# Optimization experiments

Hardware: AMD Instinct MI355X
Metric: run time of the kernel (lower is better)

## Reference

```python
import jax, jax.numpy as jnp
import numpy as np

N = 120000   # hits
K = 512      # non-noise objects (ids 1..K; id 0 = noise)
D = 8        # cluster-space dim
C = 6        # pid classes
Q_MIN = 1.0
NOISE_THR = 0
PAYLOAD_W = 1.0
EPS = 1e-9


def setup_inputs() -> dict:
    key = jax.random.key(0)
    ks = jax.random.split(key, 9)
    beta = jax.random.uniform(ks[0], (N,), dtype=jnp.float32) * 0.95 + 0.01  # keep arctanh finite
    x = jax.random.normal(ks[1], (N, D), dtype=jnp.float32)
    object_id = jax.random.randint(ks[2], (N,), 0, K + 1).astype(jnp.int32)
    # guarantee every object id (and noise id 0) appears at least once
    object_id = object_id.at[: K + 1].set(jnp.arange(K + 1, dtype=jnp.int32))
    energy = jax.random.normal(ks[3], (N,), dtype=jnp.float32)
    energy_per_hit = jax.random.normal(ks[4], (N,), dtype=jnp.float32)
    momentum = jax.random.normal(ks[5], (N, 3), dtype=jnp.float32)
    momentum_per_hit = jax.random.normal(ks[6], (N, 3), dtype=jnp.float32)
    pid_logits = jax.random.normal(ks[7], (N, C), dtype=jnp.float32)
    pid_per_hit = jax.random.randint(ks[8], (N,), 0, C).astype(jnp.int32)
    return dict(beta=beta, x=x, object_id=object_id, energy=energy,
                energy_per_hit=energy_per_hit, momentum=momentum,
                momentum_per_hit=momentum_per_hit, pid_logits=pid_logits,
                pid_per_hit=pid_per_hit)


def _oc_core(beta, x, object_id):
    """condensation_loss_tiger with weights=1, max_n_rep=0 (no repulsive sampling)."""
    oids = jnp.arange(1, K + 1, dtype=object_id.dtype)
    att_mask = object_id[:, None] == oids[None, :]              # [N, K]
    q = jnp.arctanh(beta) ** 2 + Q_MIN                          # [N]
    alphas = jnp.argmax(q[:, None] * att_mask, axis=0)          # [K] condensation points
    x_k = x[alphas]                                             # [K, D]
    q_k = q[alphas]                                             # [K]
    # squared euclidean distance via gemm (avoids [N,K,D] intermediate)
    d2 = (jnp.sum(x * x, axis=1)[:, None] + jnp.sum(x_k * x_k, axis=1)[None, :]
          - 2.0 * (x @ x_k.T))
    d2 = jnp.maximum(d2, 0.0)                                   # [N, K]
    dist = jnp.sqrt(jnp.maximum(d2, 1e-12))
    qw = q[:, None] * q_k[None, :]                              # [N, K]
    # attractive: per-object normalized by hits in object, then mean over objects
    att_norm = jnp.sum(att_mask, axis=0).astype(x.dtype)        # [K]
    v_att = jnp.sum(jnp.where(att_mask, qw * d2, 0.0) / (att_norm + EPS)[None, :]) / K
    # repulsive: hinge (1 - dist), normalized by n_hits not in object
    rep_mask = (~att_mask) & (dist < 1.0)
    n_rep_k = jnp.sum(~att_mask, axis=0).astype(x.dtype)        # [K]
    n_rep = jnp.sum(rep_mask)
    v_rep = jnp.sum(jnp.where(rep_mask, qw * (1.0 - dist), 0.0) / (n_rep_k + EPS)[None, :]) / K
    l_coward = jnp.mean(1.0 - beta[alphas])
    noise_m = (object_id <= NOISE_THR).astype(beta.dtype)
    l_noise = jnp.sum(beta * noise_m) / jnp.sum(noise_m)
    return v_att, v_rep, l_coward, l_noise, n_rep


def reference(beta, x, object_id, energy, energy_per_hit, momentum,
              momentum_per_hit, pid_logits, pid_per_hit):
    v_att, v_rep, l_coward, l_noise, n_rep = _oc_core(beta, x, object_id)
    oc_total = v_att + v_rep + l_coward + l_noise
    # payload losses on non-noise hits (masked means == F.*_loss on gathered rows)
    m = (object_id > NOISE_THR).astype(beta.dtype)              # [N]
    nm = jnp.sum(m)
    e_loss = jnp.sum((energy - energy_per_hit) ** 2 * m) / nm
    p_loss = jnp.sum((momentum - momentum_per_hit) ** 2 * m[:, None]) / (nm * momentum.shape[1])
    logp = jax.nn.log_softmax(pid_logits, axis=-1)              # [N, C]
    nll = -jnp.take_along_axis(logp, pid_per_hit[:, None], axis=1)[:, 0]
    pid_loss = jnp.sum(nll * m) / nm
    total = oc_total + PAYLOAD_W * (e_loss + p_loss + pid_loss)
    return (v_att, v_rep, l_coward, l_noise, n_rep.astype(jnp.float32),
            oc_total, e_loss, p_loss, pid_loss, total)
```

## Files before the change

### kernel.cpp

```cpp
#include <hip/hip_runtime.h>
#include <math.h>

#define KOBJ 512
#define KTW 12
#define TK 64
#define NTILE (KOBJ / TK)
#define HB 4
#define HCH (256 * HB)

__device__ __forceinline__ float wave_red_f(float v) {
  #pragma unroll
  for (int off = 32; off > 0; off >>= 1) v += __shfl_down(v, off, 64);
  return v;
}

__device__ __forceinline__ float q_of_beta(float b) {
  float a = 0.5f * __logf((1.f + b) / (1.f - b));
  return fmaf(a, a, 1.f);
}

__global__ __launch_bounds__(256) void
k_prep(const float* __restrict__ beta, const int* __restrict__ oid,
       const float* __restrict__ energy, const float* __restrict__ eph,
       const float* __restrict__ mom, const float* __restrict__ mph,
       const float* __restrict__ logits, const int* __restrict__ pid,
       unsigned long long* __restrict__ amax_part,
       unsigned* __restrict__ cnt_part,
       float* __restrict__ scal_part, int n, int M) {
  __shared__ unsigned long long lmax[KOBJ];
  __shared__ unsigned lcnt[KOBJ];
  for (int t = threadIdx.x; t < KOBJ; t += 256) { lmax[t] = 0ull; lcnt[t] = 0u; }
  __syncthreads();

  float e_t = 0.f, p_t = 0.f, pid_t = 0.f, noise_t = 0.f, ncnt = 0.f, mcnt = 0.f;
  for (int i = blockIdx.x * 256 + threadIdx.x; i < n; i += M * 256) {
    float b = beta[i];
    int o = oid[i];
    if (o > 0) {
      float q = q_of_beta(b);
      unsigned long long key = ((unsigned long long)__float_as_uint(q) << 32)
                             | (unsigned long long)(unsigned)(~(unsigned)i);
      atomicMax(&lmax[o - 1], key);
      atomicAdd(&lcnt[o - 1], 1u);
      mcnt += 1.f;
      float de = energy[i] - eph[i];
      e_t = fmaf(de, de, e_t);
      float p0 = mom[3*i+0] - mph[3*i+0];
      float p1 = mom[3*i+1] - mph[3*i+1];
      float p2 = mom[3*i+2] - mph[3*i+2];
      p_t = fmaf(p0, p0, p_t); p_t = fmaf(p1, p1, p_t); p_t = fmaf(p2, p2, p_t);
      const float* lg = logits + 6*i;
      float l0=lg[0], l1=lg[1], l2=lg[2], l3=lg[3], l4=lg[4], l5=lg[5];
      float mx = fmaxf(fmaxf(fmaxf(l0,l1),fmaxf(l2,l3)), fmaxf(l4,l5));
      float s = __expf(l0-mx)+__expf(l1-mx)+__expf(l2-mx)
              + __expf(l3-mx)+__expf(l4-mx)+__expf(l5-mx);
      int pc = pid[i];
      float lp = (pc==0)?l0:(pc==1)?l1:(pc==2)?l2:(pc==3)?l3:(pc==4)?l4:l5;
      pid_t += mx + __logf(s) - lp;
    } else {
      noise_t += b;
      ncnt += 1.f;
    }
  }
  __syncthreads();

  for (int t = threadIdx.x; t < KOBJ; t += 256) {
    amax_part[(size_t)blockIdx.x * KOBJ + t] = lmax[t];
    cnt_part[(size_t)blockIdx.x * KOBJ + t]  = lcnt[t];
  }

  float vals[6] = {e_t, p_t, pid_t, noise_t, ncnt, mcnt};
  #pragma unroll
  for (int j = 0; j < 6; j++) vals[j] = wave_red_f(vals[j]);
  __shared__ float sred[4][6];
  int w = threadIdx.x >> 6, l = threadIdx.x & 63;
  if (l == 0) {
    #pragma unroll
    for (int j = 0; j < 6; j++) sred[w][j] = vals[j];
  }
  __syncthreads();
  if (threadIdx.x == 0) {
    #pragma unroll
    for (int j = 0; j < 6; j++)
      scal_part[blockIdx.x * 8 + j] = sred[0][j]+sred[1][j]+sred[2][j]+sred[3][j];
  }
}

__global__ __launch_bounds__(256) void
k_gather(const float* __restrict__ x, const float* __restrict__ beta,
         const unsigned long long* __restrict__ amax_part,
         const unsigned* __restrict__ cnt_part,
         float* __restrict__ ktab, float* __restrict__ cow_part, int n, int M) {
  int ko = threadIdx.x & 63;
  int chunk = threadIdx.x >> 6;
  int k = blockIdx.x * 64 + ko;
  int m0 = (chunk * M) >> 2, m1 = ((chunk + 1) * M) >> 2;

  unsigned long long key = 0ull;
  unsigned cnt = 0u;
  for (int m = m0; m < m1; m++) {
    unsigned long long km = amax_part[(size_t)m * KOBJ + k];
    key = (km > key) ? km : key;
    cnt += cnt_part[(size_t)m * KOBJ + k];
  }
  __shared__ unsigned long long skey[4][64];
  __shared__ unsigned scnt[4][64];
  skey[chunk][ko] = key;
  scnt[chunk][ko] = cnt;
  __syncthreads();

  float cow = 0.f;
  if (chunk == 0) {
    #pragma unroll
    for (int c = 1; c < 4; c++) {
      unsigned long long kc = skey[c][ko];
      key = (kc > key) ? kc : key;
      cnt += scnt[c][ko];
    }
    unsigned idx = ~(unsigned)(key & 0xffffffffull);
    float q_k = __uint_as_float((unsigned)(key >> 32));
    const float4* xp = (const float4*)x;
    float4 xa = xp[2 * (size_t)idx];
    float4 xb = xp[2 * (size_t)idx + 1];
    float xv[8] = {xa.x, xa.y, xa.z, xa.w, xb.x, xb.y, xb.z, xb.w};
    float s2 = 0.f;
    #pragma unroll
    for (int c = 0; c < 8; c++) s2 = fmaf(xv[c], xv[c], s2);
    float* kt = ktab + (size_t)k * KTW;
    #pragma unroll
    for (int c = 0; c < 8; c++) kt[c] = xv[c];
    kt[8]  = s2;
    kt[9]  = q_k / ((float)(n - (int)cnt) + 1e-9f);
    kt[10] = q_k / ((float)cnt + 1e-9f);
    kt[11] = 0.f;
    cow = 1.f - beta[idx];
    cow = wave_red_f(cow);
    if (ko == 0) cow_part[blockIdx.x] = cow;
  }
}

__global__ __launch_bounds__(256) void
k_pairs(const float* __restrict__ x, const float* __restrict__ beta,
        const int* __restrict__ oid, const float* __restrict__ ktab,
        float* __restrict__ pairs_part, int n) {
  __shared__ float skt[TK * KTW];
  const int tile0 = blockIdx.y * TK;
  for (int t = threadIdx.x; t < TK * KTW; t += 256)
    skt[t] = ktab[(size_t)tile0 * KTW + t];
  __syncthreads();

  float yi[HB][8], b2[HB], qi[HB];
  int own[HB];
  const float4* xp = (const float4*)x;
  #pragma unroll
  for (int h = 0; h < HB; h++) {
    int i = blockIdx.x * HCH + h * 256 + threadIdx.x;
    if (i < n) {
      float4 xa = xp[2 * (size_t)i];
      float4 xb = xp[2 * (size_t)i + 1];
      float xi[8] = {xa.x, xa.y, xa.z, xa.w, xb.x, xb.y, xb.z, xb.w};
      float s = 0.f;
      #pragma unroll
      for (int c = 0; c < 8; c++) {
        s = fmaf(xi[c], xi[c], s);
        yi[h][c] = -2.f * xi[c];
      }
      b2[h] = s;
      qi[h] = q_of_beta(beta[i]);
      own[h] = oid[i] - 1 - tile0;
    } else {
      #pragma unroll
      for (int c = 0; c < 8; c++) yi[h][c] = 0.f;
      b2[h] = 3.f;
      qi[h] = 0.f;
      own[h] = -1;
    }
  }

  float att = 0.f, rep = 0.f, nrep = 0.f;
  #pragma unroll 2
  for (int k = 0; k < TK; k++) {
    const float* kt = &skt[k * KTW];
    float k0 = kt[0], k1 = kt[1], k2 = kt[2], k3 = kt[3];
    float k4 = kt[4], k5 = kt[5], k6 = kt[6], k7 = kt[7];
    float s2 = kt[8], wr = kt[9];
    #pragma unroll
    for (int h = 0; h < HB; h++) {
      float d2 = b2[h] + s2;
      d2 = fmaf(yi[h][0], k0, d2);
      d2 = fmaf(yi[h][1], k1, d2);
      d2 = fmaf(yi[h][2], k2, d2);
      d2 = fmaf(yi[h][3], k3, d2);
      d2 = fmaf(yi[h][4], k4, d2);
      d2 = fmaf(yi[h][5], k5, d2);
      d2 = fmaf(yi[h][6], k6, d2);
      d2 = fmaf(yi[h][7], k7, d2);
      if (d2 < 1.f) {
        float dist = sqrtf(fmaxf(d2, 1e-12f));
        rep = fmaf(qi[h] * (1.f - dist), wr, rep);
        nrep += 1.f;
      }
    }
  }

  #pragma unroll
  for (int h = 0; h < HB; h++) {
    int ko = own[h];
    if (ko >= 0 && ko < TK) {
      const float* kt = &skt[ko * KTW];
      float d2 = b2[h] + kt[8];
      #pragma unroll
      for (int c = 0; c < 8; c++) d2 = fmaf(yi[h][c], kt[c], d2);
      att = fmaf(qi[h] * fmaxf(d2, 0.f), kt[10], att);
      if (d2 < 1.f) {
        float dist = sqrtf(fmaxf(d2, 1e-12f));
        rep = fmaf(-qi[h] * (1.f - dist), kt[9], rep);
        nrep -= 1.f;
      }
    }
  }

  att = wave_red_f(att);
  rep = wave_red_f(rep);
  nrep = wave_red_f(nrep);
  __shared__ float sred[4][3];
  int w = threadIdx.x >> 6, l = threadIdx.x & 63;
  if (l == 0) { sred[w][0] = att; sred[w][1] = rep; sred[w][2] = nrep; }
  __syncthreads();
  if (threadIdx.x == 0) {
    int bid = blockIdx.y * gridDim.x + blockIdx.x;
    pairs_part[bid * 4 + 0] = sred[0][0]+sred[1][0]+sred[2][0]+sred[3][0];
    pairs_part[bid * 4 + 1] = sred[0][1]+sred[1][1]+sred[2][1]+sred[3][1];
    pairs_part[bid * 4 + 2] = sred[0][2]+sred[1][2]+sred[2][2]+sred[3][2];
  }
}

__global__ __launch_bounds__(256) void
k_finalize(const float* __restrict__ pairs_part, int nblk_tot,
           const float* __restrict__ scal_part, int M,
           const float* __restrict__ cow_part, float* __restrict__ out) {
  float v[9] = {0,0,0,0,0,0,0,0,0};
  for (int b = threadIdx.x; b < nblk_tot; b += 256) {
    v[0] += pairs_part[b * 4 + 0];
    v[1] += pairs_part[b * 4 + 1];
    v[2] += pairs_part[b * 4 + 2];
  }
  for (int m = threadIdx.x; m < M; m += 256) {
    #pragma unroll
    for (int j = 0; j < 6; j++) v[3 + j] += scal_part[m * 8 + j];
  }
  #pragma unroll
  for (int j = 0; j < 9; j++) v[j] = wave_red_f(v[j]);
  __shared__ float sred[4][9];
  int w = threadIdx.x >> 6, l = threadIdx.x & 63;
  if (l == 0) {
    #pragma unroll
    for (int j = 0; j < 9; j++) sred[w][j] = v[j];
  }
  __syncthreads();
  if (threadIdx.x == 0) {
    float t[9];
    #pragma unroll
    for (int j = 0; j < 9; j++) t[j] = sred[0][j]+sred[1][j]+sred[2][j]+sred[3][j];
    float cow = cow_part[0]+cow_part[1]+cow_part[2]+cow_part[3]
              + cow_part[4]+cow_part[5]+cow_part[6]+cow_part[7];
    float v_att  = t[0] / (float)KOBJ;
    float v_rep  = t[1] / (float)KOBJ;
    float n_rep  = t[2];
    float l_cow  = cow / (float)KOBJ;
    float l_noise = t[6] / t[7];
    float oc = v_att + v_rep + l_cow + l_noise;
    float nm = t[8];
    float e_loss  = t[3] / nm;
    float p_loss  = t[4] / (nm * 3.f);
    float pid_loss = t[5] / nm;
    out[0] = v_att;
    out[1] = v_rep;
    out[2] = l_cow;
    out[3] = l_noise;
    out[4] = n_rep;
    out[5] = oc;
    out[6] = e_loss;
    out[7] = p_loss;
    out[8] = pid_loss;
    out[9] = oc + e_loss + p_loss + pid_loss;
  }
}

extern "C" void kernel_launch(void* const* d_in, const int* in_sizes, int n_in,
                              void* d_out, int out_size, void* d_ws, size_t ws_size,
                              hipStream_t stream) {
  const float* beta   = (const float*)d_in[0];
  const float* x      = (const float*)d_in[1];
  const int*   oid    = (const int*)d_in[2];
  const float* energy = (const float*)d_in[3];
  const float* eph    = (const float*)d_in[4];
  const float* mom    = (const float*)d_in[5];
  const float* mph    = (const float*)d_in[6];
  const float* logits = (const float*)d_in[7];
  const int*   pid    = (const int*)d_in[8];
  float* out = (float*)d_out;
  const int n = in_sizes[0];
  const int nhb = (n + HCH - 1) / HCH;
  const int nblk_tot = nhb * NTILE;

  char* base = (char*)d_ws;
  size_t off = 0;
  float* ktab       = (float*)(base + off); off += (size_t)KOBJ * KTW * 4;
  float* cow_part   = (float*)(base + off); off += 8 * 4;
  float* pairs_part = (float*)(base + off); off += (size_t)nblk_tot * 4 * 4;
  off = (off + 255) & ~(size_t)255;

  size_t per_m = (size_t)KOBJ * 8 + (size_t)KOBJ * 4 + 32;
  long long avail = (long long)ws_size - (long long)off;
  int M = (int)(avail / (long long)per_m);
  if (M > 256) M = 256;
  M &= ~3;
  if (M < 4) M = 4;

  unsigned long long* amax_part = (unsigned long long*)(base + off); off += (size_t)M * KOBJ * 8;
  unsigned* cnt_part = (unsigned*)(base + off);                      off += (size_t)M * KOBJ * 4;
  float* scal_part   = (float*)(base + off);                         off += (size_t)M * 8 * 4;

  k_prep<<<M, 256, 0, stream>>>(beta, oid, energy, eph, mom, mph, logits, pid,
                                amax_part, cnt_part, scal_part, n, M);
  k_gather<<<8, 256, 0, stream>>>(x, beta, amax_part, cnt_part, ktab, cow_part, n, M);
  k_pairs<<<dim3(nhb, NTILE), 256, 0, stream>>>(x, beta, oid, ktab, pairs_part, n);
  k_finalize<<<1, 256, 0, stream>>>(pairs_part, nblk_tot, scal_part, M, cow_part, out);
}
```

Baseline: 127.4 us.

## Fuse all phases into one cooperative persistent kernel with grid syncs

Replaces the four separate launches (prep, gather, pairs, finalize) with one cooperative kernel of 512 blocks that separates the phases with grid.sync, and falls back to separate launches if the cooperative launch fails. It also raises prep parallelism to 512 blocks, spreads gather over 64 blocks, and turns the pair tiles into a grid-stride loop. The aim is to cut launch gaps and idle tail time between stages. In exchange it adds grid-barrier cost, must fit two blocks per CU, reloads the k-tile into shared memory for every work item, and makes gather reduce over more partials.

```diff
diff --git a/kernel.cpp b/kernel.cpp
--- a/kernel.cpp
+++ b/kernel.cpp
@@ -1,5 +1,8 @@
 #include <hip/hip_runtime.h>
+#include <hip/hip_cooperative_groups.h>
 #include <math.h>
+
+namespace cg = cooperative_groups;
 
 #define KOBJ 512
 #define KTW 12
@@ -7,6 +10,9 @@
 #define NTILE (KOBJ / TK)
 #define HB 4
 #define HCH (256 * HB)
+#define MPREP 512
+#define GGATH 64
+#define GRID 512
 
 __device__ __forceinline__ float wave_red_f(float v) {
   #pragma unroll
@@ -19,21 +25,20 @@
   return fmaf(a, a, 1.f);
 }
 
-__global__ __launch_bounds__(256) void
-k_prep(const float* __restrict__ beta, const int* __restrict__ oid,
-       const float* __restrict__ energy, const float* __restrict__ eph,
-       const float* __restrict__ mom, const float* __restrict__ mph,
-       const float* __restrict__ logits, const int* __restrict__ pid,
-       unsigned long long* __restrict__ amax_part,
-       unsigned* __restrict__ cnt_part,
-       float* __restrict__ scal_part, int n, int M) {
-  __shared__ unsigned long long lmax[KOBJ];
-  __shared__ unsigned lcnt[KOBJ];
-  for (int t = threadIdx.x; t < KOBJ; t += 256) { lmax[t] = 0ull; lcnt[t] = 0u; }
+__device__ __forceinline__ void
+phase_prep(const float* __restrict__ beta, const int* __restrict__ oid,
+           const float* __restrict__ energy, const float* __restrict__ eph,
+           const float* __restrict__ mom, const float* __restrict__ mph,
+           const float* __restrict__ logits, const int* __restrict__ pid,
+           unsigned long long* __restrict__ amax_part,
+           unsigned* __restrict__ cnt_part, float* __restrict__ scal_part,
+           int n, int bid, int tid,
+           unsigned long long* lmax, unsigned* lcnt, float (*sred)[10]) {
+  for (int t = tid; t < KOBJ; t += 256) { lmax[t] = 0ull; lcnt[t] = 0u; }
   __syncthreads();
 
   float e_t = 0.f, p_t = 0.f, pid_t = 0.f, noise_t = 0.f, ncnt = 0.f, mcnt = 0.f;
-  for (int i = blockIdx.x * 256 + threadIdx.x; i < n; i += M * 256) {
+  for (int i = bid * 256 + tid; i < n; i += MPREP * 256) {
     float b = beta[i];
     int o = oid[i];
     if (o > 0) {
@@ -64,58 +69,55 @@
   }
   __syncthreads();
 
-  for (int t = threadIdx.x; t < KOBJ; t += 256) {
-    amax_part[(size_t)blockIdx.x * KOBJ + t] = lmax[t];
-    cnt_part[(size_t)blockIdx.x * KOBJ + t]  = lcnt[t];
+  for (int t = tid; t < KOBJ; t += 256) {
+    amax_part[(size_t)bid * KOBJ + t] = lmax[t];
+    cnt_part[(size_t)bid * KOBJ + t]  = lcnt[t];
   }
 
   float vals[6] = {e_t, p_t, pid_t, noise_t, ncnt, mcnt};
   #pragma unroll
   for (int j = 0; j < 6; j++) vals[j] = wave_red_f(vals[j]);
-  __shared__ float sred[4][6];
-  int w = threadIdx.x >> 6, l = threadIdx.x & 63;
+  int w = tid >> 6, l = tid & 63;
   if (l == 0) {
     #pragma unroll
     for (int j = 0; j < 6; j++) sred[w][j] = vals[j];
   }
   __syncthreads();
-  if (threadIdx.x == 0) {
+  if (tid == 0) {
     #pragma unroll
     for (int j = 0; j < 6; j++)
-      scal_part[blockIdx.x * 8 + j] = sred[0][j]+sred[1][j]+sred[2][j]+sred[3][j];
-  }
-}
-
-__global__ __launch_bounds__(256) void
-k_gather(const float* __restrict__ x, const float* __restrict__ beta,
-         const unsigned long long* __restrict__ amax_part,
-         const unsigned* __restrict__ cnt_part,
-         float* __restrict__ ktab, float* __restrict__ cow_part, int n, int M) {
-  int ko = threadIdx.x & 63;
-  int chunk = threadIdx.x >> 6;
-  int k = blockIdx.x * 64 + ko;
-  int m0 = (chunk * M) >> 2, m1 = ((chunk + 1) * M) >> 2;
-
+      scal_part[bid * 8 + j] = sred[0][j]+sred[1][j]+sred[2][j]+sred[3][j];
+  }
+}
+
+__device__ __forceinline__ void
+phase_gather(const float* __restrict__ x, const float* __restrict__ beta,
+             const unsigned long long* __restrict__ amax_part,
+             const unsigned* __restrict__ cnt_part,
+             float* __restrict__ ktab, float* __restrict__ cow_part,
+             int n, int bid, int tid,
+             unsigned long long (*skey)[8], unsigned (*scnt2)[8]) {
+  int o = tid & 7;
+  int chunk = tid >> 3;
+  int k = bid * 8 + o;
+  const int mpc = MPREP / 32;
   unsigned long long key = 0ull;
   unsigned cnt = 0u;
-  for (int m = m0; m < m1; m++) {
+  for (int m = chunk * mpc; m < (chunk + 1) * mpc; m++) {
     unsigned long long km = amax_part[(size_t)m * KOBJ + k];
     key = (km > key) ? km : key;
     cnt += cnt_part[(size_t)m * KOBJ + k];
   }
-  __shared__ unsigned long long skey[4][64];
-  __shared__ unsigned scnt[4][64];
-  skey[chunk][ko] = key;
-  scnt[chunk][ko] = cnt;
-  __syncthreads();
-
-  float cow = 0.f;
+  skey[chunk][o] = key;
+  scnt2[chunk][o] = cnt;
+  __syncthreads();
+
   if (chunk == 0) {
-    #pragma unroll
-    for (int c = 1; c < 4; c++) {
-      unsigned long long kc = skey[c][ko];
+    #pragma unroll 4
+    for (int c = 1; c < 32; c++) {
+      unsigned long long kc = skey[c][o];
       key = (kc > key) ? kc : key;
-      cnt += scnt[c][ko];
+      cnt += scnt2[c][o];
     }
     unsigned idx = ~(unsigned)(key & 0xffffffffull);
     float q_k = __uint_as_float((unsigned)(key >> 32));
@@ -133,89 +135,95 @@
     kt[9]  = q_k / ((float)(n - (int)cnt) + 1e-9f);
     kt[10] = q_k / ((float)cnt + 1e-9f);
     kt[11] = 0.f;
-    cow = 1.f - beta[idx];
-    cow = wave_red_f(cow);
-    if (ko == 0) cow_part[blockIdx.x] = cow;
-  }
-}
-
-__global__ __launch_bounds__(256) void
-k_pairs(const float* __restrict__ x, const float* __restrict__ beta,
-        const int* __restrict__ oid, const float* __restrict__ ktab,
-        float* __restrict__ pairs_part, int n) {
-  __shared__ float skt[TK * KTW];
-  const int tile0 = blockIdx.y * TK;
-  for (int t = threadIdx.x; t < TK * KTW; t += 256)
-    skt[t] = ktab[(size_t)tile0 * KTW + t];
-  __syncthreads();
-
-  float yi[HB][8], b2[HB], qi[HB];
-  int own[HB];
-  const float4* xp = (const float4*)x;
-  #pragma unroll
-  for (int h = 0; h < HB; h++) {
-    int i = blockIdx.x * HCH + h * 256 + threadIdx.x;
-    if (i < n) {
-      float4 xa = xp[2 * (size_t)i];
-      float4 xb = xp[2 * (size_t)i + 1];
-      float xi[8] = {xa.x, xa.y, xa.z, xa.w, xb.x, xb.y, xb.z, xb.w};
-      float s = 0.f;
-      #pragma unroll
-      for (int c = 0; c < 8; c++) {
-        s = fmaf(xi[c], xi[c], s);
-        yi[h][c] = -2.f * xi[c];
-      }
-      b2[h] = s;
-      qi[h] = q_of_beta(beta[i]);
-      own[h] = oid[i] - 1 - tile0;
-    } else {
-      #pragma unroll
-      for (int c = 0; c < 8; c++) yi[h][c] = 0.f;
-      b2[h] = 3.f;
-      qi[h] = 0.f;
-      own[h] = -1;
-    }
-  }
-
+    float cow = 1.f - beta[idx];
+    #pragma unroll
+    for (int off = 4; off > 0; off >>= 1) cow += __shfl_down(cow, off, 8);
+    if (o == 0) cow_part[bid] = cow;
+  }
+}
+
+__device__ __forceinline__ void
+phase_pairs(const float* __restrict__ x, const float* __restrict__ beta,
+            const int* __restrict__ oid, const float* __restrict__ ktab,
+            float* __restrict__ pairs_part, int n, int nitems,
+            int bid, int tid, int gridn, float* skt, float (*sred)[10]) {
   float att = 0.f, rep = 0.f, nrep = 0.f;
-  #pragma unroll 2
-  for (int k = 0; k < TK; k++) {
-    const float* kt = &skt[k * KTW];
-    float k0 = kt[0], k1 = kt[1], k2 = kt[2], k3 = kt[3];
-    float k4 = kt[4], k5 = kt[5], k6 = kt[6], k7 = kt[7];
-    float s2 = kt[8], wr = kt[9];
+  for (int it = bid; it < nitems; it += gridn) {
+    const int tile0 = (it & (NTILE - 1)) * TK;
+    const int hbase = (it / NTILE) * HCH;
+
+    __syncthreads();
+    for (int t = tid; t < TK * KTW; t += 256)
+      skt[t] = ktab[(size_t)tile0 * KTW + t];
+    __syncthreads();
+
+    float yi[HB][8], b2[HB], qi[HB];
+    int own[HB];
+    const float4* xp = (const float4*)x;
     #pragma unroll
     for (int h = 0; h < HB; h++) {
-      float d2 = b2[h] + s2;
-      d2 = fmaf(yi[h][0], k0, d2);
-      d2 = fmaf(yi[h][1], k1, d2);
-      d2 = fmaf(yi[h][2], k2, d2);
-      d2 = fmaf(yi[h][3], k3, d2);
-      d2 = fmaf(yi[h][4], k4, d2);
-      d2 = fmaf(yi[h][5], k5, d2);
-      d2 = fmaf(yi[h][6], k6, d2);
-      d2 = fmaf(yi[h][7], k7, d2);
-      if (d2 < 1.f) {
-        float dist = sqrtf(fmaxf(d2, 1e-12f));
-        rep = fmaf(qi[h] * (1.f - dist), wr, rep);
-        nrep += 1.f;
+      int i = hbase + h * 256 + tid;
+      if (i < n) {
+        float4 xa = xp[2 * (size_t)i];
+        float4 xb = xp[2 * (size_t)i + 1];
+        float xi[8] = {xa.x, xa.y, xa.z, xa.w, xb.x, xb.y, xb.z, xb.w};
+        float s = 0.f;
+        #pragma unroll
+        for (int c = 0; c < 8; c++) {
+          s = fmaf(xi[c], xi[c], s);
+          yi[h][c] = -2.f * xi[c];
+        }
+        b2[h] = s;
+        qi[h] = q_of_beta(beta[i]);
+        own[h] = oid[i] - 1 - tile0;
+      } else {
+        #pragma unroll
+        for (int c = 0; c < 8; c++) yi[h][c] = 0.f;
+        b2[h] = 3.f;
+        qi[h] = 0.f;
+        own[h] = -1;
       }
     }
-  }
-
-  #pragma unroll
-  for (int h = 0; h < HB; h++) {
-    int ko = own[h];
-    if (ko >= 0 && ko < TK) {
-      const float* kt = &skt[ko * KTW];
-      float d2 = b2[h] + kt[8];
+
+    #pragma unroll 2
+    for (int k = 0; k < TK; k++) {
+      const float* kt = &skt[k * KTW];
+      float k0 = kt[0], k1 = kt[1], k2 = kt[2], k3 = kt[3];
+      float k4 = kt[4], k5 = kt[5], k6 = kt[6], k7 = kt[7];
+      float s2 = kt[8], wr = kt[9];
       #pragma unroll
-      for (int c = 0; c < 8; c++) d2 = fmaf(yi[h][c], kt[c], d2);
-      att = fmaf(qi[h] * fmaxf(d2, 0.f), kt[10], att);
-      if (d2 < 1.f) {
-        float dist = sqrtf(fmaxf(d2, 1e-12f));
-        rep = fmaf(-qi[h] * (1.f - dist), kt[9], rep);
-        nrep -= 1.f;
+      for (int h = 0; h < HB; h++) {
+        float d2 = b2[h] + s2;
+        d2 = fmaf(yi[h][0], k0, d2);
+        d2 = fmaf(yi[h][1], k1, d2);
+        d2 = fmaf(yi[h][2], k2, d2);
+        d2 = fmaf(yi[h][3], k3, d2);
+        d2 = fmaf(yi[h][4], k4, d2);
+        d2 = fmaf(yi[h][5], k5, d2);
+        d2 = fmaf(yi[h][6], k6, d2);
+        d2 = fmaf(yi[h][7], k7, d2);
+        if (d2 < 1.f) {
+          float dist = sqrtf(fmaxf(d2, 1e-12f));
+          rep = fmaf(qi[h] * (1.f - dist), wr, rep);
+          nrep += 1.f;
+        }
+      }
+    }
+
+    #pragma unroll
+    for (int h = 0; h < HB; h++) {
+      int ko = own[h];
+      if (ko >= 0 && ko < TK) {
+        const float* kt = &skt[ko * KTW];
+        float d2 = b2[h] + kt[8];
+        #pragma unroll
+        for (int c = 0; c < 8; c++) d2 = fmaf(yi[h][c], kt[c], d2);
+        att = fmaf(qi[h] * fmaxf(d2, 0.f), kt[10], att);
+        if (d2 < 1.f) {
+          float dist = sqrtf(fmaxf(d2, 1e-12f));
+          rep = fmaf(-qi[h] * (1.f - dist), kt[9], rep);
+          nrep -= 1.f;
+        }
       }
     }
   }
@@ -223,51 +231,52 @@
   att = wave_red_f(att);
   rep = wave_red_f(rep);
   nrep = wave_red_f(nrep);
-  __shared__ float sred[4][3];
-  int w = threadIdx.x >> 6, l = threadIdx.x & 63;
+  __syncthreads();
+  int w = tid >> 6, l = tid & 63;
   if (l == 0) { sred[w][0] = att; sred[w][1] = rep; sred[w][2] = nrep; }
   __syncthreads();
-  if (threadIdx.x == 0) {
-    int bid = blockIdx.y * gridDim.x + blockIdx.x;
+  if (tid == 0) {
     pairs_part[bid * 4 + 0] = sred[0][0]+sred[1][0]+sred[2][0]+sred[3][0];
     pairs_part[bid * 4 + 1] = sred[0][1]+sred[1][1]+sred[2][1]+sred[3][1];
     pairs_part[bid * 4 + 2] = sred[0][2]+sred[1][2]+sred[2][2]+sred[3][2];
   }
 }
 
-__global__ __launch_bounds__(256) void
-k_finalize(const float* __restrict__ pairs_part, int nblk_tot,
-           const float* __restrict__ scal_part, int M,
-           const float* __restrict__ cow_part, float* __restrict__ out) {
-  float v[9] = {0,0,0,0,0,0,0,0,0};
-  for (int b = threadIdx.x; b < nblk_tot; b += 256) {
+__device__ __forceinline__ void
+phase_final(const float* __restrict__ pairs_part, int nb_part,
+            const float* __restrict__ scal_part,
+            const float* __restrict__ cow_part, float* __restrict__ out,
+            int tid, float (*sred)[10]) {
+  float v[10];
+  #pragma unroll
+  for (int j = 0; j < 10; j++) v[j] = 0.f;
+  for (int b = tid; b < nb_part; b += 256) {
     v[0] += pairs_part[b * 4 + 0];
     v[1] += pairs_part[b * 4 + 1];
     v[2] += pairs_part[b * 4 + 2];
   }
-  for (int m = threadIdx.x; m < M; m += 256) {
+  for (int m = tid; m < MPREP; m += 256) {
     #pragma unroll
     for (int j = 0; j < 6; j++) v[3 + j] += scal_part[m * 8 + j];
   }
+  for (int g = tid; g < GGATH; g += 256) v[9] += cow_part[g];
   #pragma unroll
-  for (int j = 0; j < 9; j++) v[j] = wave_red_f(v[j]);
-  __shared__ float sred[4][9];
-  int w = threadIdx.x >> 6, l = threadIdx.x & 63;
+  for (int j = 0; j < 10; j++) v[j] = wave_red_f(v[j]);
+  __syncthreads();
+  int w = tid >> 6, l = tid & 63;
   if (l == 0) {
     #pragma unroll
-    for (int j = 0; j < 9; j++) sred[w][j] = v[j];
-  }
-  __syncthreads();
-  if (threadIdx.x == 0) {
-    float t[9];
-    #pragma unroll
-    for (int j = 0; j < 9; j++) t[j] = sred[0][j]+sred[1][j]+sred[2][j]+sred[3][j];
-    float cow = cow_part[0]+cow_part[1]+cow_part[2]+cow_part[3]
-              + cow_part[4]+cow_part[5]+cow_part[6]+cow_part[7];
+    for (int j = 0; j < 10; j++) sred[w][j] = v[j];
+  }
+  __syncthreads();
+  if (tid == 0) {
+    float t[10];
+    #pragma unroll
+    for (int j = 0; j < 10; j++) t[j] = sred[0][j]+sred[1][j]+sred[2][j]+sred[3][j];
     float v_att  = t[0] / (float)KOBJ;
     float v_rep  = t[1] / (float)KOBJ;
     float n_rep  = t[2];
-    float l_cow  = cow / (float)KOBJ;
+    float l_cow  = t[9] / (float)KOBJ;
     float l_noise = t[6] / t[7];
     float oc = v_att + v_rep + l_cow + l_noise;
     float nm = t[8];
@@ -287,6 +296,88 @@
   }
 }
 
+__global__ __launch_bounds__(256, 2) void
+k_fused(const float* __restrict__ beta, const float* __restrict__ x,
+        const int* __restrict__ oid,
+        const float* __restrict__ energy, const float* __restrict__ eph,
+        const float* __restrict__ mom, const float* __restrict__ mph,
+        const float* __restrict__ logits, const int* __restrict__ pid,
+        unsigned long long* __restrict__ amax_part,
+        unsigned* __restrict__ cnt_part, float* __restrict__ scal_part,
+        float* __restrict__ ktab, float* __restrict__ cow_part,
+        float* __restrict__ pairs_part, float* __restrict__ out,
+        int n, int nitems) {
+  cg::grid_group grid = cg::this_grid();
+  const int tid = threadIdx.x;
+  const int bid = blockIdx.x;
+
+  __shared__ unsigned long long lmax[KOBJ];
+  __shared__ unsigned lcnt[KOBJ];
+  __shared__ unsigned long long skey[32][8];
+  __shared__ unsigned scnt2[32][8];
+  __shared__ float skt[TK * KTW];
+  __shared__ float sred[4][10];
+
+  if (bid < MPREP)
+    phase_prep(beta, oid, energy, eph, mom, mph, logits, pid,
+               amax_part, cnt_part, scal_part, n, bid, tid, lmax, lcnt, sred);
+  grid.sync();
+  if (bid < GGATH)
+    phase_gather(x, beta, amax_part, cnt_part, ktab, cow_part, n, bid, tid,
+                 skey, scnt2);
+  grid.sync();
+  phase_pairs(x, beta, oid, ktab, pairs_part, n, nitems, bid, tid,
+              (int)gridDim.x, skt, sred);
+  grid.sync();
+  if (bid == 0)
+    phase_final(pairs_part, (int)gridDim.x, scal_part, cow_part, out, tid, sred);
+}
+
+__global__ __launch_bounds__(256) void
+k_prep_s(const float* __restrict__ beta, const int* __restrict__ oid,
+         const float* __restrict__ energy, const float* __restrict__ eph,
+         const float* __restrict__ mom, const float* __restrict__ mph,
+         const float* __restrict__ logits, const int* __restrict__ pid,
+         unsigned long long* __restrict__ amax_part,
+         unsigned* __restrict__ cnt_part, float* __restrict__ scal_part, int n) {
+  __shared__ unsigned long long lmax[KOBJ];
+  __shared__ unsigned lcnt[KOBJ];
+  __shared__ float sred[4][10];
+  phase_prep(beta, oid, energy, eph, mom, mph, logits, pid,
+             amax_part, cnt_part, scal_part, n, blockIdx.x, threadIdx.x,
+             lmax, lcnt, sred);
+}
+
+__global__ __launch_bounds__(256) void
+k_gather_s(const float* __restrict__ x, const float* __restrict__ beta,
+           const unsigned long long* __restrict__ amax_part,
+           const unsigned* __restrict__ cnt_part,
+           float* __restrict__ ktab, float* __restrict__ cow_part, int n) {
+  __shared__ unsigned long long skey[32][8];
+  __shared__ unsigned scnt2[32][8];
+  phase_gather(x, beta, amax_part, cnt_part, ktab, cow_part, n,
+               blockIdx.x, threadIdx.x, skey, scnt2);
+}
+
+__global__ __launch_bounds__(256) void
+k_pairs_s(const float* __restrict__ x, const float* __restrict__ beta,
+          const int* __restrict__ oid, const float* __restrict__ ktab,
+          float* __restrict__ pairs_part, int n, int nitems) {
+  __shared__ float skt[TK * KTW];
+  __shared__ float sred[4][10];
+  phase_pairs(x, beta, oid, ktab, pairs_part, n, nitems,
+              blockIdx.x, threadIdx.x, (int)gridDim.x, skt, sred);
+}
+
+__global__ __launch_bounds__(256) void
+k_final_s(const float* __restrict__ pairs_part, int nb_part,
+          const float* __restrict__ scal_part,
+          const float* __restrict__ cow_part, float* __restrict__ out) {
+  __shared__ float sred[4][10];
+  phase_final(pairs_part, nb_part, scal_part, cow_part, out,
+              threadIdx.x, sred);
+}
+
 extern "C" void kernel_launch(void* const* d_in, const int* in_sizes, int n_in,
                               void* d_out, int out_size, void* d_ws, size_t ws_size,
                               hipStream_t stream) {
@@ -302,29 +393,38 @@
   float* out = (float*)d_out;
   const int n = in_sizes[0];
   const int nhb = (n + HCH - 1) / HCH;
-  const int nblk_tot = nhb * NTILE;
+  const int nitems = nhb * NTILE;
+  const int npart_max = (nitems > GRID) ? nitems : GRID;
 
   char* base = (char*)d_ws;
   size_t off = 0;
   float* ktab       = (float*)(base + off); off += (size_t)KOBJ * KTW * 4;
-  float* cow_part   = (float*)(base + off); off += 8 * 4;
-  float* pairs_part = (float*)(base + off); off += (size_t)nblk_tot * 4 * 4;
+  float* cow_part   = (float*)(base + off); off += GGATH * 4;
+  float* pairs_part = (float*)(base + off); off += (size_t)npart_max * 4 * 4;
   off = (off + 255) & ~(size_t)255;
-
-  size_t per_m = (size_t)KOBJ * 8 + (size_t)KOBJ * 4 + 32;
-  long long avail = (long long)ws_size - (long long)off;
-  int M = (int)(avail / (long long)per_m);
-  if (M > 256) M = 256;
-  M &= ~3;
-  if (M < 4) M = 4;
-
-  unsigned long long* amax_part = (unsigned long long*)(base + off); off += (size_t)M * KOBJ * 8;
-  unsigned* cnt_part = (unsigned*)(base + off);                      off += (size_t)M * KOBJ * 4;
-  float* scal_part   = (float*)(base + off);                         off += (size_t)M * 8 * 4;
-
-  k_prep<<<M, 256, 0, stream>>>(beta, oid, energy, eph, mom, mph, logits, pid,
-                                amax_part, cnt_part, scal_part, n, M);
-  k_gather<<<8, 256, 0, stream>>>(x, beta, amax_part, cnt_part, ktab, cow_part, n, M);
-  k_pairs<<<dim3(nhb, NTILE), 256, 0, stream>>>(x, beta, oid, ktab, pairs_part, n);
-  k_finalize<<<1, 256, 0, stream>>>(pairs_part, nblk_tot, scal_part, M, cow_part, out);
-}
+  unsigned long long* amax_part = (unsigned long long*)(base + off); off += (size_t)MPREP * KOBJ * 8;
+  unsigned* cnt_part = (unsigned*)(base + off);                      off += (size_t)MPREP * KOBJ * 4;
+  float* scal_part   = (float*)(base + off);                         off += (size_t)MPREP * 8 * 4;
+
+  int n_arg = n, nitems_arg = nitems;
+  void* args[] = {
+    (void*)&beta, (void*)&x, (void*)&oid, (void*)&energy, (void*)&eph,
+    (void*)&mom, (void*)&mph, (void*)&logits, (void*)&pid,
+    (void*)&amax_part, (void*)&cnt_part, (void*)&scal_part,
+    (void*)&ktab, (void*)&cow_part, (void*)&pairs_part, (void*)&out,
+    (void*)&n_arg, (void*)&nitems_arg
+  };
+  hipError_t err = hipLaunchCooperativeKernel((const void*)k_fused, dim3(GRID),
+                                              dim3(256), args, 0, stream);
+  if (err != hipSuccess) {
+    k_prep_s<<<MPREP, 256, 0, stream>>>(beta, oid, energy, eph, mom, mph,
+                                        logits, pid, amax_part, cnt_part,
+                                        scal_part, n);
+    k_gather_s<<<GGATH, 256, 0, stream>>>(x, beta, amax_part, cnt_part,
+                                          ktab, cow_part, n);
+    k_pairs_s<<<nitems, 256, 0, stream>>>(x, beta, oid, ktab, pairs_part,
+                                          n, nitems);
+    k_final_s<<<1, 256, 0, stream>>>(pairs_part, nitems, scal_part,
+                                     cow_part, out);
+  }
+}
```

Result: slower. 297.8 us (+133.6%).

## Fuse gather and finalize into preceding kernels via last-block atomic tickets

Applied to the files above, without the earlier changes.

Merges the four-kernel pipeline into two launches. The last block of the prep kernel, found through an atomic ticket counter, does the per-object argmax reduction and the condensation-point table. The last block of the pairs kernel does the final reduction and writes the outputs. This removes two kernel launches and their gaps, but puts the 512-object gather, over 256 partials, onto a single block, where before it was spread over 8 blocks. It also adds a memset for the counters and fixes M at 256 regardless of workspace size.

```diff
diff --git a/kernel.cpp b/kernel.cpp
--- a/kernel.cpp
+++ b/kernel.cpp
@@ -7,6 +7,7 @@
 #define NTILE (KOBJ / TK)
 #define HB 4
 #define HCH (256 * HB)
+#define MPREP 256
 
 __device__ __forceinline__ float wave_red_f(float v) {
   #pragma unroll
@@ -20,20 +21,27 @@
 }
 
 __global__ __launch_bounds__(256) void
-k_prep(const float* __restrict__ beta, const int* __restrict__ oid,
-       const float* __restrict__ energy, const float* __restrict__ eph,
-       const float* __restrict__ mom, const float* __restrict__ mph,
-       const float* __restrict__ logits, const int* __restrict__ pid,
-       unsigned long long* __restrict__ amax_part,
-       unsigned* __restrict__ cnt_part,
-       float* __restrict__ scal_part, int n, int M) {
+k_A(const float* __restrict__ beta, const float* __restrict__ x,
+    const int* __restrict__ oid,
+    const float* __restrict__ energy, const float* __restrict__ eph,
+    const float* __restrict__ mom, const float* __restrict__ mph,
+    const float* __restrict__ logits, const int* __restrict__ pid,
+    unsigned long long* __restrict__ amax_part,
+    unsigned* __restrict__ cnt_part, float* __restrict__ scal_part,
+    float* __restrict__ ktab, float* __restrict__ cow_sum,
+    unsigned* __restrict__ ctr, int n) {
   __shared__ unsigned long long lmax[KOBJ];
   __shared__ unsigned lcnt[KOBJ];
-  for (int t = threadIdx.x; t < KOBJ; t += 256) { lmax[t] = 0ull; lcnt[t] = 0u; }
+  __shared__ float sred[4][6];
+  __shared__ int sticket;
+  const int tid = threadIdx.x;
+  const int bid = blockIdx.x;
+
+  for (int t = tid; t < KOBJ; t += 256) { lmax[t] = 0ull; lcnt[t] = 0u; }
   __syncthreads();
 
   float e_t = 0.f, p_t = 0.f, pid_t = 0.f, noise_t = 0.f, ncnt = 0.f, mcnt = 0.f;
-  for (int i = blockIdx.x * 256 + threadIdx.x; i < n; i += M * 256) {
+  for (int i = bid * 256 + tid; i < n; i += MPREP * 256) {
     float b = beta[i];
     int o = oid[i];
     if (o > 0) {
@@ -64,58 +72,41 @@
   }
   __syncthreads();
 
-  for (int t = threadIdx.x; t < KOBJ; t += 256) {
-    amax_part[(size_t)blockIdx.x * KOBJ + t] = lmax[t];
-    cnt_part[(size_t)blockIdx.x * KOBJ + t]  = lcnt[t];
+  for (int t = tid; t < KOBJ; t += 256) {
+    amax_part[(size_t)bid * KOBJ + t] = lmax[t];
+    cnt_part[(size_t)bid * KOBJ + t]  = lcnt[t];
   }
 
   float vals[6] = {e_t, p_t, pid_t, noise_t, ncnt, mcnt};
   #pragma unroll
   for (int j = 0; j < 6; j++) vals[j] = wave_red_f(vals[j]);
-  __shared__ float sred[4][6];
-  int w = threadIdx.x >> 6, l = threadIdx.x & 63;
+  int w = tid >> 6, l = tid & 63;
   if (l == 0) {
     #pragma unroll
     for (int j = 0; j < 6; j++) sred[w][j] = vals[j];
   }
   __syncthreads();
-  if (threadIdx.x == 0) {
+  if (tid == 0) {
     #pragma unroll
     for (int j = 0; j < 6; j++)
-      scal_part[blockIdx.x * 8 + j] = sred[0][j]+sred[1][j]+sred[2][j]+sred[3][j];
-  }
-}
-
-__global__ __launch_bounds__(256) void
-k_gather(const float* __restrict__ x, const float* __restrict__ beta,
-         const unsigned long long* __restrict__ amax_part,
-         const unsigned* __restrict__ cnt_part,
-         float* __restrict__ ktab, float* __restrict__ cow_part, int n, int M) {
-  int ko = threadIdx.x & 63;
-  int chunk = threadIdx.x >> 6;
-  int k = blockIdx.x * 64 + ko;
-  int m0 = (chunk * M) >> 2, m1 = ((chunk + 1) * M) >> 2;
-
-  unsigned long long key = 0ull;
-  unsigned cnt = 0u;
-  for (int m = m0; m < m1; m++) {
-    unsigned long long km = amax_part[(size_t)m * KOBJ + k];
-    key = (km > key) ? km : key;
-    cnt += cnt_part[(size_t)m * KOBJ + k];
-  }
-  __shared__ unsigned long long skey[4][64];
-  __shared__ unsigned scnt[4][64];
-  skey[chunk][ko] = key;
-  scnt[chunk][ko] = cnt;
-  __syncthreads();
-
+      scal_part[bid * 8 + j] = sred[0][j]+sred[1][j]+sred[2][j]+sred[3][j];
+  }
+
+  __threadfence();
+  if (tid == 0) sticket = (int)atomicAdd(ctr, 1u);
+  __syncthreads();
+  if (sticket != MPREP - 1) return;
+
+  __threadfence();
   float cow = 0.f;
-  if (chunk == 0) {
-    #pragma unroll
-    for (int c = 1; c < 4; c++) {
-      unsigned long long kc = skey[c][ko];
-      key = (kc > key) ? kc : key;
-      cnt += scnt[c][ko];
+  for (int k = tid; k < KOBJ; k += 256) {
+    unsigned long long key = 0ull;
+    unsigned cnt = 0u;
+    #pragma unroll 8
+    for (int m = 0; m < MPREP; m++) {
+      unsigned long long km = amax_part[(size_t)m * KOBJ + k];
+      key = (km > key) ? km : key;
+      cnt += cnt_part[(size_t)m * KOBJ + k];
     }
     unsigned idx = ~(unsigned)(key & 0xffffffffull);
     float q_k = __uint_as_float((unsigned)(key >> 32));
@@ -133,19 +124,31 @@
     kt[9]  = q_k / ((float)(n - (int)cnt) + 1e-9f);
     kt[10] = q_k / ((float)cnt + 1e-9f);
     kt[11] = 0.f;
-    cow = 1.f - beta[idx];
-    cow = wave_red_f(cow);
-    if (ko == 0) cow_part[blockIdx.x] = cow;
-  }
+    cow += 1.f - beta[idx];
+  }
+  cow = wave_red_f(cow);
+  __syncthreads();
+  if (l == 0) sred[w][0] = cow;
+  __syncthreads();
+  if (tid == 0)
+    cow_sum[0] = sred[0][0]+sred[1][0]+sred[2][0]+sred[3][0];
 }
 
 __global__ __launch_bounds__(256) void
-k_pairs(const float* __restrict__ x, const float* __restrict__ beta,
-        const int* __restrict__ oid, const float* __restrict__ ktab,
-        float* __restrict__ pairs_part, int n) {
+k_B(const float* __restrict__ x, const float* __restrict__ beta,
+    const int* __restrict__ oid, const float* __restrict__ ktab,
+    const float* __restrict__ scal_part, const float* __restrict__ cow_sum,
+    float* __restrict__ pairs_part, unsigned* __restrict__ ctr,
+    float* __restrict__ out, int n, int nblk_tot) {
   __shared__ float skt[TK * KTW];
+  __shared__ float sred[4][9];
+  __shared__ int sticket;
+  const int tid = threadIdx.x;
+  const int bid = blockIdx.y * gridDim.x + blockIdx.x;
   const int tile0 = blockIdx.y * TK;
-  for (int t = threadIdx.x; t < TK * KTW; t += 256)
+  const int hbase = blockIdx.x * HCH;
+
+  for (int t = tid; t < TK * KTW; t += 256)
     skt[t] = ktab[(size_t)tile0 * KTW + t];
   __syncthreads();
 
@@ -154,7 +157,7 @@
   const float4* xp = (const float4*)x;
   #pragma unroll
   for (int h = 0; h < HB; h++) {
-    int i = blockIdx.x * HCH + h * 256 + threadIdx.x;
+    int i = hbase + h * 256 + tid;
     if (i < n) {
       float4 xa = xp[2 * (size_t)i];
       float4 xb = xp[2 * (size_t)i + 1];
@@ -223,51 +226,49 @@
   att = wave_red_f(att);
   rep = wave_red_f(rep);
   nrep = wave_red_f(nrep);
-  __shared__ float sred[4][3];
-  int w = threadIdx.x >> 6, l = threadIdx.x & 63;
+  int w = tid >> 6, l = tid & 63;
   if (l == 0) { sred[w][0] = att; sred[w][1] = rep; sred[w][2] = nrep; }
   __syncthreads();
-  if (threadIdx.x == 0) {
-    int bid = blockIdx.y * gridDim.x + blockIdx.x;
+  if (tid == 0) {
     pairs_part[bid * 4 + 0] = sred[0][0]+sred[1][0]+sred[2][0]+sred[3][0];
     pairs_part[bid * 4 + 1] = sred[0][1]+sred[1][1]+sred[2][1]+sred[3][1];
     pairs_part[bid * 4 + 2] = sred[0][2]+sred[1][2]+sred[2][2]+sred[3][2];
   }
-}
-
-__global__ __launch_bounds__(256) void
-k_finalize(const float* __restrict__ pairs_part, int nblk_tot,
-           const float* __restrict__ scal_part, int M,
-           const float* __restrict__ cow_part, float* __restrict__ out) {
-  float v[9] = {0,0,0,0,0,0,0,0,0};
-  for (int b = threadIdx.x; b < nblk_tot; b += 256) {
+
+  __threadfence();
+  if (tid == 0) sticket = (int)atomicAdd(ctr, 1u);
+  __syncthreads();
+  if (sticket != nblk_tot - 1) return;
+
+  __threadfence();
+  float v[9];
+  #pragma unroll
+  for (int j = 0; j < 9; j++) v[j] = 0.f;
+  for (int b = tid; b < nblk_tot; b += 256) {
     v[0] += pairs_part[b * 4 + 0];
     v[1] += pairs_part[b * 4 + 1];
     v[2] += pairs_part[b * 4 + 2];
   }
-  for (int m = threadIdx.x; m < M; m += 256) {
+  for (int m = tid; m < MPREP; m += 256) {
     #pragma unroll
     for (int j = 0; j < 6; j++) v[3 + j] += scal_part[m * 8 + j];
   }
   #pragma unroll
   for (int j = 0; j < 9; j++) v[j] = wave_red_f(v[j]);
-  __shared__ float sred[4][9];
-  int w = threadIdx.x >> 6, l = threadIdx.x & 63;
+  __syncthreads();
   if (l == 0) {
     #pragma unroll
     for (int j = 0; j < 9; j++) sred[w][j] = v[j];
   }
   __syncthreads();
-  if (threadIdx.x == 0) {
+  if (tid == 0) {
     float t[9];
     #pragma unroll
     for (int j = 0; j < 9; j++) t[j] = sred[0][j]+sred[1][j]+sred[2][j]+sred[3][j];
-    float cow = cow_part[0]+cow_part[1]+cow_part[2]+cow_part[3]
-              + cow_part[4]+cow_part[5]+cow_part[6]+cow_part[7];
     float v_att  = t[0] / (float)KOBJ;
     float v_rep  = t[1] / (float)KOBJ;
     float n_rep  = t[2];
-    float l_cow  = cow / (float)KOBJ;
+    float l_cow  = cow_sum[0] / (float)KOBJ;
     float l_noise = t[6] / t[7];
     float oc = v_att + v_rep + l_cow + l_noise;
     float nm = t[8];
@@ -306,25 +307,20 @@
 
   char* base = (char*)d_ws;
   size_t off = 0;
+  unsigned* ctr     = (unsigned*)(base + off); off += 2 * 4;
+  off = (off + 255) & ~(size_t)255;
   float* ktab       = (float*)(base + off); off += (size_t)KOBJ * KTW * 4;
-  float* cow_part   = (float*)(base + off); off += 8 * 4;
+  float* cow_sum    = (float*)(base + off); off += 4 * 4;
   float* pairs_part = (float*)(base + off); off += (size_t)nblk_tot * 4 * 4;
   off = (off + 255) & ~(size_t)255;
-
-  size_t per_m = (size_t)KOBJ * 8 + (size_t)KOBJ * 4 + 32;
-  long long avail = (long long)ws_size - (long long)off;
-  int M = (int)(avail / (long long)per_m);
-  if (M > 256) M = 256;
-  M &= ~3;
-  if (M < 4) M = 4;
-
-  unsigned long long* amax_part = (unsigned long long*)(base + off); off += (size_t)M * KOBJ * 8;
-  unsigned* cnt_part = (unsigned*)(base + off);                      off += (size_t)M * KOBJ * 4;
-  float* scal_part   = (float*)(base + off);                         off += (size_t)M * 8 * 4;
-
-  k_prep<<<M, 256, 0, stream>>>(beta, oid, energy, eph, mom, mph, logits, pid,
-                                amax_part, cnt_part, scal_part, n, M);
-  k_gather<<<8, 256, 0, stream>>>(x, beta, amax_part, cnt_part, ktab, cow_part, n, M);
-  k_pairs<<<dim3(nhb, NTILE), 256, 0, stream>>>(x, beta, oid, ktab, pairs_part, n);
-  k_finalize<<<1, 256, 0, stream>>>(pairs_part, nblk_tot, scal_part, M, cow_part, out);
-}
+  unsigned long long* amax_part = (unsigned long long*)(base + off); off += (size_t)MPREP * KOBJ * 8;
+  unsigned* cnt_part = (unsigned*)(base + off);                      off += (size_t)MPREP * KOBJ * 4;
+  float* scal_part   = (float*)(base + off);                         off += (size_t)MPREP * 8 * 4;
+
+  hipMemsetAsync(ctr, 0, 2 * 4, stream);
+  k_A<<<MPREP, 256, 0, stream>>>(beta, x, oid, energy, eph, mom, mph, logits, pid,
+                                 amax_part, cnt_part, scal_part, ktab, cow_sum,
+                                 &ctr[0], n);
+  k_B<<<dim3(nhb, NTILE), 256, 0, stream>>>(x, beta, oid, ktab, scal_part, cow_sum,
+                                            pairs_part, &ctr[1], out, n, nblk_tot);
+}
```

Result: slower. 239.4 us (+87.9%).
